# Kernel tuning notes

Hardware: AMD Instinct MI355X
Metric: run time of the kernel (lower is better)

The kernel has to match this reference:

```python
import jax, jax.numpy as jnp
import numpy as np

N_LEVELS = 12
N_FEATURES = 2
HASH_SIZE = 1 << 14  # 16384
BASE_RESOLUTION = 16
PER_LEVEL_SCALE = 2.0
BATCH = 4_194_304


def _resolutions():
    # matches the torch loop: int(round(cur)) with cur *= per_level_scale
    res = []
    cur = float(BASE_RESOLUTION)
    for _ in range(N_LEVELS):
        res.append(int(round(cur)))
        cur *= PER_LEVEL_SCALE
    return jnp.asarray(res, dtype=jnp.float32)  # [L]


def setup_inputs() -> dict:
    key = jax.random.key(0)
    k1, k2 = jax.random.split(key)
    x = jax.random.uniform(k1, (BATCH,), dtype=jnp.float32)
    # learned hash table, init uniform(-1e-4, 1e-4) like the torch module
    table = jax.random.uniform(
        k2, (HASH_SIZE, N_LEVELS * N_FEATURES), dtype=jnp.float32,
        minval=-1e-4, maxval=1e-4,
    )
    return {"x": x, "table": table}


def reference(x, table):
    # x: [B] in [0,1]; table: [HASH_SIZE, L*F]
    res = _resolutions()                       # [L]
    xc = jnp.clip(x, 0.0, 1.0)                 # [B]
    pos = xc[:, None] * res[None, :]           # [B, L] -- all levels at once
    i0 = jnp.floor(pos).astype(jnp.int32)      # [B, L]
    w = (pos - i0.astype(pos.dtype))[..., None]  # [B, L, 1]
    h0 = i0 % HASH_SIZE                        # [B, L]
    h1 = (i0 + 1) % HASH_SIZE                  # [B, L]
    emb3 = table.reshape(HASH_SIZE, N_LEVELS, N_FEATURES)  # [H, L, F]
    lvl = jnp.arange(N_LEVELS)[None, :]        # [1, L]
    e0 = emb3[h0, lvl]                         # [B, L, F] gather per level
    e1 = emb3[h1, lvl]                         # [B, L, F]
    feats = (1.0 - w) * e0 + w * e1            # [B, L, F]
    # torch concatenates per-level [B,F] slices -> level-major layout
    return feats.reshape(x.shape[0], N_LEVELS * N_FEATURES)
```

## Files before the change

kernel.cpp:

```cpp
#include <hip/hip_runtime.h>

#define HASH_SIZE 16384
#define N_LEVELS  12
#define LP        6

__global__ __launch_bounds__(256) void build_ws_kernel(
    const float* __restrict__ table,
    float4* __restrict__ ws4)
{
    int tid = blockIdx.x * blockDim.x + threadIdx.x;
    if (tid >= N_LEVELS * HASH_SIZE) return;
    int l  = tid >> 14;
    int h  = tid & (HASH_SIZE - 1);
    int h1 = (h + 1) & (HASH_SIZE - 1);
    const float2 e0 = *reinterpret_cast<const float2*>(table + h  * (N_LEVELS * 2) + l * 2);
    const float2 e1 = *reinterpret_cast<const float2*>(table + h1 * (N_LEVELS * 2) + l * 2);
    ws4[tid] = make_float4(e0.x, e0.y, e1.x, e1.y);
}

__global__ __launch_bounds__(256) void hashgrid_main_kernel(
    const float* __restrict__ x,
    const float4* __restrict__ ws4,
    float4* __restrict__ out4,
    int total)
{
    int t = blockIdx.x * blockDim.x + threadIdx.x;
    if (t >= total) return;

    int b = t / LP;
    int p = t - b * LP;

    float xc = fminf(fmaxf(x[b], 0.0f), 1.0f);

    float4 r;
    #pragma unroll
    for (int k = 0; k < 2; ++k) {
        int   lvl = p * 2 + k;
        float res = (float)(16 << lvl);
        float pos = xc * res;
        float fi  = floorf(pos);
        float w   = pos - fi;
        int   h0  = ((int)fi) & (HASH_SIZE - 1);

        float4 e = ws4[lvl * HASH_SIZE + h0];

        float omw = 1.0f - w;
        float r0 = omw * e.x + w * e.z;
        float r1 = omw * e.y + w * e.w;
        if (k == 0) { r.x = r0; r.y = r1; }
        else        { r.z = r0; r.w = r1; }
    }

    out4[t] = r;
}

__global__ __launch_bounds__(256) void hashgrid_direct_kernel(
    const float* __restrict__ x,
    const float* __restrict__ table,
    float* __restrict__ out,
    int total)
{
    int idx = blockIdx.x * blockDim.x + threadIdx.x;
    if (idx >= total) return;
    int b = idx / N_LEVELS;
    int l = idx - b * N_LEVELS;
    float xc  = fminf(fmaxf(x[b], 0.0f), 1.0f);
    float res = (float)(16 << l);
    float pos = xc * res;
    float fi  = floorf(pos);
    int   i0  = (int)fi;
    float w   = pos - fi;
    int h0 = i0 & (HASH_SIZE - 1);
    int h1 = (i0 + 1) & (HASH_SIZE - 1);
    const float2 e0 = *reinterpret_cast<const float2*>(table + h0 * (N_LEVELS * 2) + l * 2);
    const float2 e1 = *reinterpret_cast<const float2*>(table + h1 * (N_LEVELS * 2) + l * 2);
    float omw = 1.0f - w;
    float2 rr;
    rr.x = omw * e0.x + w * e1.x;
    rr.y = omw * e0.y + w * e1.y;
    *reinterpret_cast<float2*>(out + (size_t)idx * 2) = rr;
}

extern "C" void kernel_launch(void* const* d_in, const int* in_sizes, int n_in,
                              void* d_out, int out_size, void* d_ws, size_t ws_size,
                              hipStream_t stream) {
    const float* x     = (const float*)d_in[0];
    const float* table = (const float*)d_in[1];
    int batch = in_sizes[0];

    const size_t ws_needed = (size_t)N_LEVELS * HASH_SIZE * sizeof(float4);

    if (ws_size >= ws_needed) {
        float4* ws4 = (float4*)d_ws;

        int ta = N_LEVELS * HASH_SIZE;
        build_ws_kernel<<<(ta + 255) / 256, 256, 0, stream>>>(table, ws4);

        int total = batch * LP;
        hashgrid_main_kernel<<<(total + 255) / 256, 256, 0, stream>>>(
            x, ws4, (float4*)d_out, total);
    } else {
        int total = batch * N_LEVELS;
        hashgrid_direct_kernel<<<(total + 255) / 256, 256, 0, stream>>>(
            x, table, (float*)d_out, total);
    }
}
```

Before: 506.7 us.

## Stage coarse hash levels in LDS and use persistent grid-stride loop

```diff
diff --git a/kernel.cpp b/kernel.cpp
--- a/kernel.cpp
+++ b/kernel.cpp
@@ -3,6 +3,10 @@
 #define HASH_SIZE 16384
 #define N_LEVELS  12
 #define LP        6
+#define NSTAGED   6
+#define LDS_TOT   1014
+
+typedef float floatx4 __attribute__((ext_vector_type(4)));
 
 __global__ __launch_bounds__(256) void build_ws_kernel(
     const float* __restrict__ table,
@@ -21,37 +25,61 @@
 __global__ __launch_bounds__(256) void hashgrid_main_kernel(
     const float* __restrict__ x,
     const float4* __restrict__ ws4,
-    float4* __restrict__ out4,
+    float* __restrict__ out,
     int total)
 {
-    int t = blockIdx.x * blockDim.x + threadIdx.x;
-    if (t >= total) return;
+    __shared__ float4 lds[LDS_TOT];
 
+    #pragma unroll
+    for (int l = 0; l < NSTAGED; ++l) {
+        const int off = (l == 0) ? 0 : (l == 1) ? 17 : (l == 2) ? 50
+                      : (l == 3) ? 115 : (l == 4) ? 244 : 501;
+        const int n   = (16 << l) + 1;
+        for (int h = threadIdx.x; h < n; h += 256)
+            lds[off + h] = ws4[l * HASH_SIZE + h];
+    }
+    __syncthreads();
+
+    const int stride = gridDim.x * 256;
+    int t = blockIdx.x * 256 + threadIdx.x;
     int b = t / LP;
-    int p = t - b * LP;
+    const int p = t - b * LP;
+    const int bstep = stride / LP;
 
-    float xc = fminf(fmaxf(x[b], 0.0f), 1.0f);
+    const int   l0 = 2 * p, l1 = 2 * p + 1;
+    const float res0 = (float)(16 << l0);
+    const float res1 = (float)(16 << l1);
+    const bool  inLds = (p < 3);
+    const int lo0 = (p == 0) ? 0  : (p == 1) ? 50  : 244;
+    const int lo1 = (p == 0) ? 17 : (p == 1) ? 115 : 501;
+    const float4* g0 = ws4 + l0 * HASH_SIZE;
+    const float4* g1 = ws4 + l1 * HASH_SIZE;
 
-    float4 r;
-    #pragma unroll
-    for (int k = 0; k < 2; ++k) {
-        int   lvl = p * 2 + k;
-        float res = (float)(16 << lvl);
-        float pos = xc * res;
-        float fi  = floorf(pos);
-        float w   = pos - fi;
-        int   h0  = ((int)fi) & (HASH_SIZE - 1);
+    #pragma unroll 2
+    for (; t < total; t += stride, b += bstep) {
+        float xc = fminf(fmaxf(x[b], 0.0f), 1.0f);
+        float p0 = xc * res0, p1 = xc * res1;
+        float f0 = floorf(p0), f1 = floorf(p1);
+        float w0 = p0 - f0,    w1 = p1 - f1;
+        int   h0 = (int)f0,    h1 = (int)f1;
 
-        float4 e = ws4[lvl * HASH_SIZE + h0];
+        float4 e0, e1;
+        if (inLds) {
+            e0 = lds[lo0 + h0];
+            e1 = lds[lo1 + h1];
+        } else {
+            e0 = g0[h0 & (HASH_SIZE - 1)];
+            e1 = g1[h1 & (HASH_SIZE - 1)];
+        }
 
-        float omw = 1.0f - w;
-        float r0 = omw * e.x + w * e.z;
-        float r1 = omw * e.y + w * e.w;
-        if (k == 0) { r.x = r0; r.y = r1; }
-        else        { r.z = r0; r.w = r1; }
+        floatx4 r;
+        r.x = (1.0f - w0) * e0.x + w0 * e0.z;
+        r.y = (1.0f - w0) * e0.y + w0 * e0.w;
+        r.z = (1.0f - w1) * e1.x + w1 * e1.z;
+        r.w = (1.0f - w1) * e1.y + w1 * e1.w;
+
+        __builtin_nontemporal_store(r, reinterpret_cast<floatx4*>(out) + t);
     }
-
-    out4[t] = r;
 }
 
 __global__ __launch_bounds__(256) void hashgrid_direct_kernel(
@@ -97,8 +125,9 @@
         build_ws_kernel<<<(ta + 255) / 256, 256, 0, stream>>>(table, ws4);
 
         int total = batch * LP;
-        hashgrid_main_kernel<<<(total + 255) / 256, 256, 0, stream>>>(
-            x, ws4, (float4*)d_out, total);
+        int grid = 3072;
+        hashgrid_main_kernel<<<grid, 256, 0, stream>>>(
+            x, ws4, (float*)d_out, total);
     } else {
         int total = batch * N_LEVELS;
         hashgrid_direct_kernel<<<(total + 255) / 256, 256, 0, stream>>>(
```

After: 515.8 us. About the same (+1.8%).

## Stage mid-resolution levels in LDS and use persistent grid-stride blocks with nontemporal I/O

Applied to the files above, without the earlier changes.

```diff
diff --git a/kernel.cpp b/kernel.cpp
--- a/kernel.cpp
+++ b/kernel.cpp
@@ -3,6 +3,13 @@
 #define HASH_SIZE 16384
 #define N_LEVELS  12
 #define LP        6
+
+#define L6_OFF 0
+#define L7_OFF 1026
+#define L8_OFF 3076
+#define LDS_N  7174
+
+typedef float floatx4 __attribute__((ext_vector_type(4)));
 
 __global__ __launch_bounds__(256) void build_ws_kernel(
     const float* __restrict__ table,
@@ -18,21 +25,108 @@
     ws4[tid] = make_float4(e0.x, e0.y, e1.x, e1.y);
 }
 
-__global__ __launch_bounds__(256) void hashgrid_main_kernel(
+__global__ __launch_bounds__(768, 6) void hashgrid_lds_kernel(
     const float* __restrict__ x,
     const float4* __restrict__ ws4,
-    float4* __restrict__ out4,
+    float* __restrict__ out,
+    int quarter)
+{
+    __shared__ float2 lds2[LDS_N];
+
+    for (int i = threadIdx.x; i < LDS_N; i += 768) {
+        int l, off;
+        if      (i < L7_OFF) { l = 6; off = L6_OFF; }
+        else if (i < L8_OFF) { l = 7; off = L7_OFF; }
+        else                 { l = 8; off = L8_OFF; }
+        float4 e = ws4[l * HASH_SIZE + (i - off)];
+        lds2[i] = make_float2(e.x, e.y);
+    }
+    __syncthreads();
+
+    const int stride = gridDim.x * 768;
+    int t = blockIdx.x * 768 + threadIdx.x;
+    int b = t / LP;
+    const int p = t - b * LP;
+    const int bstep = stride / LP;
+    const int bq = quarter / LP;
+
+    const int   la = 2 * p, lb = la + 1;
+    const float resa = (float)(16 << la);
+    const float resb = (float)(16 << lb);
+    const float4* __restrict__ ga = ws4 + la * HASH_SIZE;
+    const float4* __restrict__ gb = ws4 + lb * HASH_SIZE;
+    const floatx4* __restrict__ gan = reinterpret_cast<const floatx4*>(ga);
+    const floatx4* __restrict__ gbn = reinterpret_cast<const floatx4*>(gb);
+    floatx4* __restrict__ out4 = reinterpret_cast<floatx4*>(out);
+
+    for (; t < quarter; t += stride, b += bstep) {
+        int   ha[4], hb[4];
+        float wa[4], wb[4];
+        #pragma unroll
+        for (int q = 0; q < 4; ++q) {
+            float xc = fminf(fmaxf(x[b + q * bq], 0.0f), 1.0f);
+            float pa = xc * resa, pb = xc * resb;
+            float fa = floorf(pa), fb = floorf(pb);
+            wa[q] = pa - fa;  wb[q] = pb - fb;
+            ha[q] = ((int)fa) & (HASH_SIZE - 1);
+            hb[q] = ((int)fb) & (HASH_SIZE - 1);
+        }
+
+        float4 ea[4], eb[4];
+        if (p < 3) {
+            #pragma unroll
+            for (int q = 0; q < 4; ++q) { ea[q] = ga[ha[q]]; eb[q] = gb[hb[q]]; }
+        } else if (p == 3) {
+            #pragma unroll
+            for (int q = 0; q < 4; ++q) {
+                float2 a0 = lds2[L6_OFF + ha[q]], a1 = lds2[L6_OFF + ha[q] + 1];
+                float2 b0 = lds2[L7_OFF + hb[q]], b1 = lds2[L7_OFF + hb[q] + 1];
+                ea[q] = make_float4(a0.x, a0.y, a1.x, a1.y);
+                eb[q] = make_float4(b0.x, b0.y, b1.x, b1.y);
+            }
+        } else if (p == 4) {
+            #pragma unroll
+            for (int q = 0; q < 4; ++q) {
+                float2 a0 = lds2[L8_OFF + ha[q]], a1 = lds2[L8_OFF + ha[q] + 1];
+                ea[q] = make_float4(a0.x, a0.y, a1.x, a1.y);
+                floatx4 v = __builtin_nontemporal_load(gbn + hb[q]);
+                eb[q] = make_float4(v.x, v.y, v.z, v.w);
+            }
+        } else {
+            #pragma unroll
+            for (int q = 0; q < 4; ++q) {
+                floatx4 va = __builtin_nontemporal_load(gan + ha[q]);
+                floatx4 vb = __builtin_nontemporal_load(gbn + hb[q]);
+                ea[q] = make_float4(va.x, va.y, va.z, va.w);
+                eb[q] = make_float4(vb.x, vb.y, vb.z, vb.w);
+            }
+        }
+
+        #pragma unroll
+        for (int q = 0; q < 4; ++q) {
+            floatx4 r;
+            r.x = (1.0f - wa[q]) * ea[q].x + wa[q] * ea[q].z;
+            r.y = (1.0f - wa[q]) * ea[q].y + wa[q] * ea[q].w;
+            r.z = (1.0f - wb[q]) * eb[q].x + wb[q] * eb[q].z;
+            r.w = (1.0f - wb[q]) * eb[q].y + wb[q] * eb[q].w;
+            __builtin_nontemporal_store(r, out4 + t + q * quarter);
+        }
+    }
+}
+
+__global__ __launch_bounds__(256) void hashgrid_pair_kernel(
+    const float* __restrict__ x,
+    const float4* __restrict__ ws4,
+    float* __restrict__ out,
     int total)
 {
-    int t = blockIdx.x * blockDim.x + threadIdx.x;
+    int t = blockIdx.x * 256 + threadIdx.x;
     if (t >= total) return;
-
     int b = t / LP;
     int p = t - b * LP;
-
     float xc = fminf(fmaxf(x[b], 0.0f), 1.0f);
 
-    float4 r;
+    floatx4 r;
     #pragma unroll
     for (int k = 0; k < 2; ++k) {
         int   lvl = p * 2 + k;
@@ -41,17 +135,14 @@
         float fi  = floorf(pos);
         float w   = pos - fi;
         int   h0  = ((int)fi) & (HASH_SIZE - 1);
-
         float4 e = ws4[lvl * HASH_SIZE + h0];
-
         float omw = 1.0f - w;
         float r0 = omw * e.x + w * e.z;
         float r1 = omw * e.y + w * e.w;
         if (k == 0) { r.x = r0; r.y = r1; }
         else        { r.z = r0; r.w = r1; }
     }
-
-    out4[t] = r;
+    __builtin_nontemporal_store(r, reinterpret_cast<floatx4*>(out) + t);
 }
 
 __global__ __launch_bounds__(256) void hashgrid_direct_kernel(
@@ -97,8 +188,14 @@
         build_ws_kernel<<<(ta + 255) / 256, 256, 0, stream>>>(table, ws4);
 
         int total = batch * LP;
-        hashgrid_main_kernel<<<(total + 255) / 256, 256, 0, stream>>>(
-            x, ws4, (float4*)d_out, total);
+        if ((batch & 3) == 0) {
+            int quarter = total >> 2;
+            hashgrid_lds_kernel<<<512, 768, 0, stream>>>(
+                x, ws4, (float*)d_out, quarter);
+        } else {
+            hashgrid_pair_kernel<<<(total + 255) / 256, 256, 0, stream>>>(
+                x, ws4, (float*)d_out, total);
+        }
     } else {
         int total = batch * N_LEVELS;
         hashgrid_direct_kernel<<<(total + 255) / 256, 256, 0, stream>>>(
```

New measurement: 588.9 us. 16.2% more time.
